# Kernel optimization log

Measured on AMD Instinct MI355X. Metric: run time of the kernel, lower is better.

The kernel has to match this reference:

```python
import jax, jax.numpy as jnp
import numpy as np

N, E, H, T = 50000, 100000, 512, 6  # nodes, edges, hidden_size, num_edge_types


def setup_inputs() -> dict:
    key = jax.random.key(0)
    ks = jax.random.split(key, 14)
    xav = 1.0 / np.sqrt(H)
    return {
        "statement_embeddings": jax.random.normal(ks[0], (N, H), jnp.float32),
        "source_indices": jax.random.randint(ks[1], (E,), 0, N, dtype=jnp.int32),
        "dest_indices": jax.random.randint(ks[2], (E,), 0, N, dtype=jnp.int32),
        "edge_types": jax.random.randint(ks[3], (E,), 0, T, dtype=jnp.int32),
        "num_nodes": N,
        "hidden_size": H,
        # edge_dense: Dense(features=6*H), xavier_uniform kernel, tiny-normal bias
        "W_edge": jax.random.uniform(ks[4], (H, T * H), jnp.float32, -1.0, 1.0) * np.sqrt(6.0 / (H + T * H)),
        "b_edge": jax.random.normal(ks[5], (T * H,), jnp.float32) * 1e-6,
        # GRUCell params (flax convention: input denses have bias; hidden r/z denses no bias; hidden n dense has bias)
        "W_ir": jax.random.normal(ks[6], (H, H), jnp.float32) * xav,
        "W_iz": jax.random.normal(ks[7], (H, H), jnp.float32) * xav,
        "W_in": jax.random.normal(ks[8], (H, H), jnp.float32) * xav,
        "b_ir": jnp.zeros((H,), jnp.float32),
        "b_iz": jnp.zeros((H,), jnp.float32),
        "b_in": jnp.zeros((H,), jnp.float32),
        "W_hr": jax.random.normal(ks[9], (H, H), jnp.float32) * xav,
        "W_hz": jax.random.normal(ks[10], (H, H), jnp.float32) * xav,
        "W_hn": jax.random.normal(ks[11], (H, H), jnp.float32) * xav,
        "b_hn": jnp.zeros((H,), jnp.float32),
    }


def reference(statement_embeddings, source_indices, dest_indices, edge_types,
              num_nodes, hidden_size,
              W_edge, b_edge,
              W_ir, W_iz, W_in, b_ir, b_iz, b_in,
              W_hr, W_hz, W_hn, b_hn):
    num_edge_types = 6
    # gather source node embeddings: [E, H]
    src = statement_embeddings[source_indices]
    # per-edge dense to all edge types: [E, T*H] -> [E, T, H]
    all_types = (src @ W_edge + b_edge).reshape(-1, num_edge_types, hidden_size)
    # select the slice for each edge's type: [E, H]
    msgs = jnp.take_along_axis(all_types, edge_types[:, None, None], axis=1)[:, 0, :]
    # scatter-add to destination nodes: [N, H]
    proposed = jax.ops.segment_sum(msgs, dest_indices, num_segments=num_nodes)
    # GRU update: inputs=proposed, carry=statement_embeddings
    h = statement_embeddings
    r = jax.nn.sigmoid(proposed @ W_ir + b_ir + h @ W_hr)
    z = jax.nn.sigmoid(proposed @ W_iz + b_iz + h @ W_hz)
    n = jnp.tanh(proposed @ W_in + b_in + r * (h @ W_hn + b_hn))
    return (1.0 - z) * n + z * h
```

## Files before the change

### kernel.cpp

```cpp
#include <hip/hip_runtime.h>
#include <hip/hip_bf16.h>
#include <math.h>

#define H 512
#define NT 6
#define BM 64
#define BN 64

typedef short bf16x8 __attribute__((ext_vector_type(8)));
typedef float f32x4 __attribute__((ext_vector_type(4)));

__device__ __forceinline__ float sigmoidf_(float x) { return 1.0f / (1.0f + expf(-x)); }

__device__ __forceinline__ unsigned short f2bf(float f) {
    unsigned int u = __float_as_uint(f);
    u = (u + 0x7FFF + ((u >> 16) & 1)) >> 16;
    return (unsigned short)u;
}
__device__ __forceinline__ float bf2f(unsigned short s) {
    unsigned int u = ((unsigned int)s) << 16;
    return __uint_as_float(u);
}

__device__ __forceinline__ void async16(const unsigned short* g, short* l) {
    __builtin_amdgcn_global_load_lds((const __attribute__((address_space(1))) void*)g,
                                     (__attribute__((address_space(3))) void*)l, 16, 0, 0);
}

__global__ void hist_kernel(const int* __restrict__ etype, int E, int* __restrict__ meta) {
    __shared__ int lh[NT];
    if (threadIdx.x < NT) lh[threadIdx.x] = 0;
    __syncthreads();
    int i = blockIdx.x * blockDim.x + threadIdx.x;
    if (i < E) atomicAdd(&lh[etype[i]], 1);
    __syncthreads();
    if (threadIdx.x < NT) {
        int c = lh[threadIdx.x];
        if (c) atomicAdd(&meta[threadIdx.x], c);
    }
}

__global__ void prefix_kernel(int* __restrict__ meta) {
    if (threadIdx.x == 0 && blockIdx.x == 0) {
        int acc = 0;
        for (int t = 0; t < NT; ++t) {
            meta[8 + t]  = acc;
            meta[16 + t] = acc;
            acc += ((meta[t] + BM - 1) / BM) * BM;
        }
        meta[8 + NT] = acc;
    }
}

__global__ void scatter_perm_kernel(const int* __restrict__ etype, int E,
                                    int* __restrict__ meta, int* __restrict__ perm) {
    __shared__ int lcount[NT];
    __shared__ int lbase[NT];
    const int tid = threadIdx.x;
    if (tid < NT) lcount[tid] = 0;
    __syncthreads();
    int i = blockIdx.x * blockDim.x + tid;
    int t = 0, rank = 0;
    if (i < E) {
        t = etype[i];
        rank = atomicAdd(&lcount[t], 1);
    }
    __syncthreads();
    if (tid < NT) {
        int c = lcount[tid];
        lbase[tid] = c ? atomicAdd(&meta[16 + tid], c) : 0;
    }
    __syncthreads();
    if (i < E) perm[lbase[t] + rank] = i;
}

__global__ void node_hist_kernel(const int* __restrict__ dst, int E, int* __restrict__ cnt) {
    int i = blockIdx.x * blockDim.x + threadIdx.x;
    if (i < E) atomicAdd(&cnt[dst[i]], 1);
}

__global__ void scan1_kernel(const int* __restrict__ cnt, int n,
                             int* __restrict__ nodeStart, int* __restrict__ partials) {
    __shared__ int sh[256];
    const int tid = threadIdx.x;
    const int base = blockIdx.x * 1024 + tid * 4;
    int v[4];
    int tsum = 0;
    #pragma unroll
    for (int j = 0; j < 4; ++j) { v[j] = (base + j < n) ? cnt[base + j] : 0; tsum += v[j]; }
    sh[tid] = tsum;
    __syncthreads();
    for (int ofs = 1; ofs < 256; ofs <<= 1) {
        int add = (tid >= ofs) ? sh[tid - ofs] : 0;
        __syncthreads();
        sh[tid] += add;
        __syncthreads();
    }
    int run = sh[tid] - tsum;
    #pragma unroll
    for (int j = 0; j < 4; ++j) {
        if (base + j < n) nodeStart[base + j] = run;
        run += v[j];
    }
    if (tid == 255) partials[blockIdx.x] = sh[255];
}

__global__ void scan2_kernel(int* __restrict__ partials, int nB, int* __restrict__ nodeStart, int n) {
    if (threadIdx.x == 0 && blockIdx.x == 0) {
        int acc = 0;
        for (int b = 0; b < nB; ++b) { int t = partials[b]; partials[b] = acc; acc += t; }
        nodeStart[n] = acc;
    }
}

__global__ void scan3_kernel(int* __restrict__ nodeStart, const int* __restrict__ partials, int n) {
    int i = blockIdx.x * blockDim.x + threadIdx.x;
    if (i < n) nodeStart[i] += partials[i >> 10];
}

__global__ void slot_kernel(const int* __restrict__ dst, int E, const int* __restrict__ nodeStart,
                            int* __restrict__ cursor, int* __restrict__ destSlot) {
    int i = blockIdx.x * blockDim.x + threadIdx.x;
    if (i < E) {
        int d = dst[i];
        destSlot[i] = nodeStart[d] + atomicAdd(&cursor[d], 1);
    }
}

__global__ void conv_bf16_kernel(const float* __restrict__ in, unsigned short* __restrict__ out, int n4) {
    int i = blockIdx.x * blockDim.x + threadIdx.x;
    if (i < n4) {
        float4 v = ((const float4*)in)[i];
        ushort4 o;
        o.x = f2bf(v.x); o.y = f2bf(v.y); o.z = f2bf(v.z); o.w = f2bf(v.w);
        ((ushort4*)out)[i] = o;
    }
}

__global__ void conv_gru_w_kernel(const float* __restrict__ Wir, const float* __restrict__ Wiz,
                                  const float* __restrict__ Win, const float* __restrict__ Whr,
                                  const float* __restrict__ Whz, const float* __restrict__ Whn,
                                  unsigned short* __restrict__ Brt, unsigned short* __restrict__ Bzt,
                                  unsigned short* __restrict__ Bnit, unsigned short* __restrict__ Bnht) {
    int idx = blockIdx.x * blockDim.x + threadIdx.x;
    if (idx >= 512 * 1024) return;
    int n = idx >> 10;
    int k = idx & 1023;
    int kk = k & 511;
    const float* wr = (k < 512) ? Wir : Whr;
    const float* wz = (k < 512) ? Wiz : Whz;
    Brt[idx] = f2bf(wr[kk * H + n]);
    Bzt[idx] = f2bf(wz[kk * H + n]);
    if (k < 512) Bnit[n * H + k]  = f2bf(Win[k * H + n]);
    else         Bnht[n * H + kk] = f2bf(Whn[kk * H + n]);
}

__global__ void conv_edge_w_kernel(const float* __restrict__ W_edge, unsigned short* __restrict__ WeT) {
    int idx = blockIdx.x * blockDim.x + threadIdx.x;
    if (idx >= 3072 * 512) return;
    int n = idx >> 9;
    int k = idx & 511;
    WeT[idx] = f2bf(W_edge[(size_t)k * (NT * H) + n]);
}

__global__ __launch_bounds__(256)
void edge_msg_mfma2(const unsigned short* __restrict__ emb_bf,
                    const int* __restrict__ src_idx,
                    const float* __restrict__ b_edge,
                    const unsigned short* __restrict__ WeT,
                    const int* __restrict__ meta,
                    const int* __restrict__ perm,
                    const int* __restrict__ destSlot,
                    unsigned short* __restrict__ msgbuf)
{
    __shared__ __align__(16) short lds[8 * 512];
    __shared__ __align__(16) short Cs[64][72];
    __shared__ int ls_slot[BM];
    __shared__ int ls_srcb[BM];

    const int rowBase = blockIdx.y * BM;
    if (rowBase >= meta[8 + NT]) return;
    int t = 0;
    while (rowBase >= meta[8 + t + 1]) ++t;

    const int colBase = blockIdx.x * BN;
    const int tid = threadIdx.x;
    if (tid < BM) {
        int e = perm[rowBase + tid];
        ls_slot[tid] = (e >= 0) ? destSlot[e] : -1;
        ls_srcb[tid] = (e >= 0) ? src_idx[e] * H : 0;
    }
    __syncthreads();

    const int lane = tid & 63;
    const int wv = tid >> 6;
    const int r = lane & 15;
    const int q = lane >> 4;
    const int wm = (wv >> 1) * 32;
    const int wn = (wv & 1) * 32;

    const unsigned short* pg[2];
    #pragma unroll
    for (int s = 0; s < 2; ++s) {
        int grp = wv * 2 + s;
        if (grp < 4) pg[s] = emb_bf + (size_t)ls_srcb[grp * 16 + r] + q * 8;
        else         pg[s] = WeT + ((size_t)(t * H + colBase + (grp - 4) * 16 + r)) * H + q * 8;
    }
    short* ld0 = &lds[(wv * 2) * 512];
    short* ld1 = &lds[(wv * 2 + 1) * 512];

    f32x4 acc[2][2];
    #pragma unroll
    for (int i = 0; i < 2; ++i)
        #pragma unroll
        for (int j = 0; j < 2; ++j) acc[i][j] = (f32x4){0.f, 0.f, 0.f, 0.f};

    for (int ks = 0; ks < 16; ++ks) {
        async16(pg[0], ld0);
        async16(pg[1], ld1);
        pg[0] += 32; pg[1] += 32;
        __syncthreads();
        bf16x8 a0 = *(const bf16x8*)&lds[(wm / 16 + 0) * 512 + lane * 8];
        bf16x8 a1 = *(const bf16x8*)&lds[(wm / 16 + 1) * 512 + lane * 8];
        bf16x8 b0 = *(const bf16x8*)&lds[(4 + wn / 16 + 0) * 512 + lane * 8];
        bf16x8 b1 = *(const bf16x8*)&lds[(4 + wn / 16 + 1) * 512 + lane * 8];
        acc[0][0] = __builtin_amdgcn_mfma_f32_16x16x32_bf16(a0, b0, acc[0][0], 0, 0, 0);
        acc[0][1] = __builtin_amdgcn_mfma_f32_16x16x32_bf16(a0, b1, acc[0][1], 0, 0, 0);
        acc[1][0] = __builtin_amdgcn_mfma_f32_16x16x32_bf16(a1, b0, acc[1][0], 0, 0, 0);
        acc[1][1] = __builtin_amdgcn_mfma_f32_16x16x32_bf16(a1, b1, acc[1][1], 0, 0, 0);
        __syncthreads();
    }

    float bias0 = b_edge[t * H + colBase + wn + r];
    float bias1 = b_edge[t * H + colBase + wn + 16 + r];
    #pragma unroll
    for (int i = 0; i < 2; ++i)
        #pragma unroll
        for (int reg = 0; reg < 4; ++reg) {
            int row = wm + i * 16 + q * 4 + reg;
            Cs[row][wn + r]      = (short)f2bf(acc[i][0][reg] + bias0);
            Cs[row][wn + 16 + r] = (short)f2bf(acc[i][1][reg] + bias1);
        }
    __syncthreads();

    int row = tid >> 2;
    int cc = (tid & 3) * 16;
    int slot = ls_slot[row];
    if (slot >= 0) {
        uint4* dst0 = (uint4*)&msgbuf[(size_t)slot * H + colBase + cc];
        dst0[0] = *(const uint4*)&Cs[row][cc];
        dst0[1] = *(const uint4*)&Cs[row][cc + 8];
    }
}

__global__ void segreduce_kernel(const unsigned short* __restrict__ msgbuf,
                                 const int* __restrict__ nodeStart,
                                 unsigned short* __restrict__ prop_bf, int N) {
    int idx = blockIdx.x * blockDim.x + threadIdx.x;
    if (idx >= N * 64) return;
    int node = idx >> 6;
    int cg = (idx & 63) * 8;
    int s0 = nodeStart[node], s1 = nodeStart[node + 1];
    float acc[8] = {0.f, 0.f, 0.f, 0.f, 0.f, 0.f, 0.f, 0.f};
    for (int s = s0; s < s1; ++s) {
        uint4 v = *(const uint4*)&msgbuf[(size_t)s * H + cg];
        const unsigned short* u = (const unsigned short*)&v;
        #pragma unroll
        for (int j = 0; j < 8; ++j) acc[j] += bf2f(u[j]);
    }
    unsigned short o[8];
    #pragma unroll
    for (int j = 0; j < 8; ++j) o[j] = f2bf(acc[j]);
    *(uint4*)&prop_bf[(size_t)node * H + cg] = *(const uint4*)o;
}

__global__ __launch_bounds__(256)
void gru_mfma2(const unsigned short* __restrict__ prop_bf,
               const unsigned short* __restrict__ emb_bf,
               const float* __restrict__ emb_f32,
               const unsigned short* __restrict__ Brt,
               const unsigned short* __restrict__ Bzt,
               const unsigned short* __restrict__ Bnit,
               const unsigned short* __restrict__ Bnht,
               const float* __restrict__ bir, const float* __restrict__ biz,
               const float* __restrict__ bin, const float* __restrict__ bhn,
               float* __restrict__ out, int N)
{
    __shared__ __align__(16) short lds[4 * 2048];

    const int tid = threadIdx.x;
    const int lane = tid & 63;
    const int wv = tid >> 6;
    const int r = lane & 15;
    const int q = lane >> 4;
    const int rowBase = blockIdx.y * BM;
    const int colBase = blockIdx.x * BN;
    const int wm = (wv >> 1) * 32;
    const int wn = (wv & 1) * 32;

    f32x4 accR[2][2], accZ[2][2], accNI[2][2], accNH[2][2];
    #pragma unroll
    for (int i = 0; i < 2; ++i)
        #pragma unroll
        for (int j = 0; j < 2; ++j) {
            accR[i][j] = (f32x4){0.f, 0.f, 0.f, 0.f};
            accZ[i][j] = accR[i][j];
            accNI[i][j] = accR[i][j];
            accNH[i][j] = accR[i][j];
        }

    short* ldsT = &lds[wv * 2048];

    for (int half = 0; half < 2; ++half) {
        const unsigned short* pg[4];
        if (wv == 0) {
            const unsigned short* s = half ? emb_bf : prop_bf;
            #pragma unroll
            for (int g = 0; g < 4; ++g)
                pg[g] = s + (size_t)(rowBase + g * 16 + r) * H + q * 8;
        } else if (wv == 1) {
            #pragma unroll
            for (int g = 0; g < 4; ++g)
                pg[g] = Brt + (size_t)(colBase + g * 16 + r) * 1024 + half * 512 + q * 8;
        } else if (wv == 2) {
            #pragma unroll
            for (int g = 0; g < 4; ++g)
                pg[g] = Bzt + (size_t)(colBase + g * 16 + r) * 1024 + half * 512 + q * 8;
        } else {
            const unsigned short* s = half ? Bnht : Bnit;
            #pragma unroll
            for (int g = 0; g < 4; ++g)
                pg[g] = s + (size_t)(colBase + g * 16 + r) * H + q * 8;
        }

        f32x4 (&accN)[2][2] = half ? accNH : accNI;

        for (int ks = 0; ks < 16; ++ks) {
            #pragma unroll
            for (int g = 0; g < 4; ++g) {
                async16(pg[g], ldsT + g * 512);
                pg[g] += 32;
            }
            __syncthreads();

            bf16x8 a0 = *(const bf16x8*)&lds[0 * 2048 + (wm / 16 + 0) * 512 + lane * 8];
            bf16x8 a1 = *(const bf16x8*)&lds[0 * 2048 + (wm / 16 + 1) * 512 + lane * 8];
            bf16x8 br0 = *(const bf16x8*)&lds[1 * 2048 + (wn / 16 + 0) * 512 + lane * 8];
            bf16x8 br1 = *(const bf16x8*)&lds[1 * 2048 + (wn / 16 + 1) * 512 + lane * 8];
            bf16x8 bz0 = *(const bf16x8*)&lds[2 * 2048 + (wn / 16 + 0) * 512 + lane * 8];
            bf16x8 bz1 = *(const bf16x8*)&lds[2 * 2048 + (wn / 16 + 1) * 512 + lane * 8];
            bf16x8 bn0 = *(const bf16x8*)&lds[3 * 2048 + (wn / 16 + 0) * 512 + lane * 8];
            bf16x8 bn1 = *(const bf16x8*)&lds[3 * 2048 + (wn / 16 + 1) * 512 + lane * 8];

            accR[0][0] = __builtin_amdgcn_mfma_f32_16x16x32_bf16(a0, br0, accR[0][0], 0, 0, 0);
            accR[0][1] = __builtin_amdgcn_mfma_f32_16x16x32_bf16(a0, br1, accR[0][1], 0, 0, 0);
            accR[1][0] = __builtin_amdgcn_mfma_f32_16x16x32_bf16(a1, br0, accR[1][0], 0, 0, 0);
            accR[1][1] = __builtin_amdgcn_mfma_f32_16x16x32_bf16(a1, br1, accR[1][1], 0, 0, 0);
            accZ[0][0] = __builtin_amdgcn_mfma_f32_16x16x32_bf16(a0, bz0, accZ[0][0], 0, 0, 0);
            accZ[0][1] = __builtin_amdgcn_mfma_f32_16x16x32_bf16(a0, bz1, accZ[0][1], 0, 0, 0);
            accZ[1][0] = __builtin_amdgcn_mfma_f32_16x16x32_bf16(a1, bz0, accZ[1][0], 0, 0, 0);
            accZ[1][1] = __builtin_amdgcn_mfma_f32_16x16x32_bf16(a1, bz1, accZ[1][1], 0, 0, 0);
            accN[0][0] = __builtin_amdgcn_mfma_f32_16x16x32_bf16(a0, bn0, accN[0][0], 0, 0, 0);
            accN[0][1] = __builtin_amdgcn_mfma_f32_16x16x32_bf16(a0, bn1, accN[0][1], 0, 0, 0);
            accN[1][0] = __builtin_amdgcn_mfma_f32_16x16x32_bf16(a1, bn0, accN[1][0], 0, 0, 0);
            accN[1][1] = __builtin_amdgcn_mfma_f32_16x16x32_bf16(a1, bn1, accN[1][1], 0, 0, 0);
            __syncthreads();
        }
    }

    #pragma unroll
    for (int i = 0; i < 2; ++i) {
        #pragma unroll
        for (int reg = 0; reg < 4; ++reg) {
            int row = rowBase + wm + i * 16 + q * 4 + reg;
            if (row >= N) continue;
            #pragma unroll
            for (int j = 0; j < 2; ++j) {
                int col = colBase + wn + j * 16 + r;
                float rg = sigmoidf_(accR[i][j][reg] + bir[col]);
                float zg = sigmoidf_(accZ[i][j][reg] + biz[col]);
                float ng = tanhf(accNI[i][j][reg] + bin[col] + rg * (accNH[i][j][reg] + bhn[col]));
                float h = emb_f32[(size_t)row * H + col];
                out[(size_t)row * H + col] = (1.0f - zg) * ng + zg * h;
            }
        }
    }
}

extern "C" void kernel_launch(void* const* d_in, const int* in_sizes, int n_in,
                              void* d_out, int out_size, void* d_ws, size_t ws_size,
                              hipStream_t stream) {
    const float* emb     = (const float*)d_in[0];
    const int*   src_idx = (const int*)d_in[1];
    const int*   dst_idx = (const int*)d_in[2];
    const int*   etype   = (const int*)d_in[3];
    const float* W_edge  = (const float*)d_in[6];
    const float* b_edge  = (const float*)d_in[7];
    const float* Wir = (const float*)d_in[8];
    const float* Wiz = (const float*)d_in[9];
    const float* Win = (const float*)d_in[10];
    const float* bir = (const float*)d_in[11];
    const float* biz = (const float*)d_in[12];
    const float* bin = (const float*)d_in[13];
    const float* Whr = (const float*)d_in[14];
    const float* Whz = (const float*)d_in[15];
    const float* Whn = (const float*)d_in[16];
    const float* bhn = (const float*)d_in[17];

    const int E = in_sizes[1];
    const int N = in_sizes[0] / H;
    const int NH = N * H;
    const int maxRowTiles = (E + BM - 1) / BM + NT;

    char* ws = (char*)d_ws;
    unsigned short* prop_bf  = (unsigned short*)ws;  ws += (size_t)NH * 2;
    unsigned short* emb_bf   = (unsigned short*)ws;  ws += (size_t)NH * 2;
    unsigned short* msgbuf   = (unsigned short*)ws;  ws += (size_t)E * H * 2;
    unsigned short* Brt      = (unsigned short*)ws;  ws += 512 * 1024 * 2;
    unsigned short* Bzt      = (unsigned short*)ws;  ws += 512 * 1024 * 2;
    unsigned short* Bnit     = (unsigned short*)ws;  ws += 512 * 512 * 2;
    unsigned short* Bnht     = (unsigned short*)ws;  ws += 512 * 512 * 2;
    unsigned short* WeT      = (unsigned short*)ws;  ws += 3072 * 512 * 2;
    int* meta      = (int*)ws;  ws += 32 * 4;
    int* typePerm  = (int*)ws;  ws += (size_t)maxRowTiles * BM * 4;
    int* nodeCnt   = (int*)ws;  ws += (size_t)N * 4;
    int* nodeStart = (int*)ws;  ws += ((size_t)N + 4) * 4;
    int* cursor    = (int*)ws;  ws += (size_t)N * 4;
    int* partials  = (int*)ws;  ws += 64 * 4;
    int* destSlot  = (int*)ws;

    hipMemsetAsync(meta, 0, 32 * 4, stream);
    hipMemsetAsync(typePerm, 0xFF, (size_t)maxRowTiles * BM * 4, stream);
    hipMemsetAsync(nodeCnt, 0, (size_t)N * 4, stream);
    hipMemsetAsync(cursor, 0, (size_t)N * 4, stream);

    const int n4 = NH / 4;
    conv_bf16_kernel<<<(n4 + 255) / 256, 256, 0, stream>>>(emb, emb_bf, n4);
    conv_gru_w_kernel<<<(512 * 1024 + 255) / 256, 256, 0, stream>>>(
        Wir, Wiz, Win, Whr, Whz, Whn, Brt, Bzt, Bnit, Bnht);
    conv_edge_w_kernel<<<(3072 * 512 + 255) / 256, 256, 0, stream>>>(W_edge, WeT);

    hist_kernel<<<(E + 255) / 256, 256, 0, stream>>>(etype, E, meta);
    prefix_kernel<<<1, 64, 0, stream>>>(meta);
    scatter_perm_kernel<<<(E + 255) / 256, 256, 0, stream>>>(etype, E, meta, typePerm);

    node_hist_kernel<<<(E + 255) / 256, 256, 0, stream>>>(dst_idx, E, nodeCnt);
    const int nB = (N + 1023) / 1024;
    scan1_kernel<<<nB, 256, 0, stream>>>(nodeCnt, N, nodeStart, partials);
    scan2_kernel<<<1, 64, 0, stream>>>(partials, nB, nodeStart, N);
    scan3_kernel<<<(N + 255) / 256, 256, 0, stream>>>(nodeStart, partials, N);
    slot_kernel<<<(E + 255) / 256, 256, 0, stream>>>(dst_idx, E, nodeStart, cursor, destSlot);

    dim3 egrid(H / BN, maxRowTiles);
    edge_msg_mfma2<<<egrid, 256, 0, stream>>>(emb_bf, src_idx, b_edge, WeT,
                                              meta, typePerm, destSlot, msgbuf);

    segreduce_kernel<<<((size_t)N * 64 + 255) / 256, 256, 0, stream>>>(msgbuf, nodeStart, prop_bf, N);

    dim3 ggrid(H / BN, (N + BM - 1) / BM);
    gru_mfma2<<<ggrid, 256, 0, stream>>>(prop_bf, emb_bf, emb, Brt, Bzt, Bnit, Bnht,
                                         bir, biz, bin, bhn, (float*)d_out, N);
}
```

Before: 940.7 us.

## Double-buffer LDS tiles in edge-message and GRU MFMA kernels

Both MFMA GEMM kernels now keep two LDS buffers and issue the async global-to-LDS copy for the next K-step before computing on the current one. This hides global load latency and drops one barrier per iteration. The GRU kernel also prefetches across the prop/emb half boundary with a fully unrolled half loop. The cost is twice the LDS per block, which may lower occupancy. Correctness depends on the async copies being complete at the single remaining barrier.

```diff
diff --git a/kernel.cpp b/kernel.cpp
--- a/kernel.cpp
+++ b/kernel.cpp
@@ -164,7 +164,7 @@
 }
 
 __global__ __launch_bounds__(256)
-void edge_msg_mfma2(const unsigned short* __restrict__ emb_bf,
+void edge_msg_mfma3(const unsigned short* __restrict__ emb_bf,
                     const int* __restrict__ src_idx,
                     const float* __restrict__ b_edge,
                     const unsigned short* __restrict__ WeT,
@@ -173,7 +173,7 @@
                     const int* __restrict__ destSlot,
                     unsigned short* __restrict__ msgbuf)
 {
-    __shared__ __align__(16) short lds[8 * 512];
+    __shared__ __align__(16) short lds[2][8 * 512];
     __shared__ __align__(16) short Cs[64][72];
     __shared__ int ls_slot[BM];
     __shared__ int ls_srcb[BM];
@@ -206,8 +206,8 @@
         if (grp < 4) pg[s] = emb_bf + (size_t)ls_srcb[grp * 16 + r] + q * 8;
         else         pg[s] = WeT + ((size_t)(t * H + colBase + (grp - 4) * 16 + r)) * H + q * 8;
     }
-    short* ld0 = &lds[(wv * 2) * 512];
-    short* ld1 = &lds[(wv * 2 + 1) * 512];
+    short* my0 = &lds[0][(wv * 2) * 512];
+    short* my1 = &lds[0][(wv * 2 + 1) * 512];
 
     f32x4 acc[2][2];
     #pragma unroll
@@ -215,21 +215,28 @@
         #pragma unroll
         for (int j = 0; j < 2; ++j) acc[i][j] = (f32x4){0.f, 0.f, 0.f, 0.f};
 
+    async16(pg[0], my0);
+    async16(pg[1], my1);
+
     for (int ks = 0; ks < 16; ++ks) {
-        async16(pg[0], ld0);
-        async16(pg[1], ld1);
-        pg[0] += 32; pg[1] += 32;
         __syncthreads();
-        bf16x8 a0 = *(const bf16x8*)&lds[(wm / 16 + 0) * 512 + lane * 8];
-        bf16x8 a1 = *(const bf16x8*)&lds[(wm / 16 + 1) * 512 + lane * 8];
-        bf16x8 b0 = *(const bf16x8*)&lds[(4 + wn / 16 + 0) * 512 + lane * 8];
-        bf16x8 b1 = *(const bf16x8*)&lds[(4 + wn / 16 + 1) * 512 + lane * 8];
+        if (ks < 15) {
+            const int off = (ks + 1) * 32;
+            const int bofs = ((ks & 1) ? 0 : 4096);
+            async16(pg[0] + off, my0 + bofs);
+            async16(pg[1] + off, my1 + bofs);
+        }
+        const short* L = &lds[ks & 1][0];
+        bf16x8 a0 = *(const bf16x8*)&L[(wm / 16 + 0) * 512 + lane * 8];
+        bf16x8 a1 = *(const bf16x8*)&L[(wm / 16 + 1) * 512 + lane * 8];
+        bf16x8 b0 = *(const bf16x8*)&L[(4 + wn / 16 + 0) * 512 + lane * 8];
+        bf16x8 b1 = *(const bf16x8*)&L[(4 + wn / 16 + 1) * 512 + lane * 8];
         acc[0][0] = __builtin_amdgcn_mfma_f32_16x16x32_bf16(a0, b0, acc[0][0], 0, 0, 0);
         acc[0][1] = __builtin_amdgcn_mfma_f32_16x16x32_bf16(a0, b1, acc[0][1], 0, 0, 0);
         acc[1][0] = __builtin_amdgcn_mfma_f32_16x16x32_bf16(a1, b0, acc[1][0], 0, 0, 0);
         acc[1][1] = __builtin_amdgcn_mfma_f32_16x16x32_bf16(a1, b1, acc[1][1], 0, 0, 0);
-        __syncthreads();
-    }
+    }
+    __syncthreads();
 
     float bias0 = b_edge[t * H + colBase + wn + r];
     float bias1 = b_edge[t * H + colBase + wn + 16 + r];
@@ -275,7 +282,7 @@
 }
 
 __global__ __launch_bounds__(256)
-void gru_mfma2(const unsigned short* __restrict__ prop_bf,
+void gru_mfma3(const unsigned short* __restrict__ prop_bf,
                const unsigned short* __restrict__ emb_bf,
                const float* __restrict__ emb_f32,
                const unsigned short* __restrict__ Brt,
@@ -286,7 +293,7 @@
                const float* __restrict__ bin, const float* __restrict__ bhn,
                float* __restrict__ out, int N)
 {
-    __shared__ __align__(16) short lds[4 * 2048];
+    __shared__ __align__(16) short lds[2][4 * 2048];
 
     const int tid = threadIdx.x;
     const int lane = tid & 63;
@@ -298,6 +305,38 @@
     const int wm = (wv >> 1) * 32;
     const int wn = (wv & 1) * 32;
 
+    const unsigned short* h0[4];
+    const unsigned short* h1[4];
+    if (wv == 0) {
+        #pragma unroll
+        for (int g = 0; g < 4; ++g) {
+            size_t rowoff = (size_t)(rowBase + g * 16 + r) * H + q * 8;
+            h0[g] = prop_bf + rowoff;
+            h1[g] = emb_bf + rowoff;
+        }
+    } else if (wv == 1) {
+        #pragma unroll
+        for (int g = 0; g < 4; ++g) {
+            h0[g] = Brt + (size_t)(colBase + g * 16 + r) * 1024 + q * 8;
+            h1[g] = h0[g] + 512;
+        }
+    } else if (wv == 2) {
+        #pragma unroll
+        for (int g = 0; g < 4; ++g) {
+            h0[g] = Bzt + (size_t)(colBase + g * 16 + r) * 1024 + q * 8;
+            h1[g] = h0[g] + 512;
+        }
+    } else {
+        #pragma unroll
+        for (int g = 0; g < 4; ++g) {
+            size_t coloff = (size_t)(colBase + g * 16 + r) * H + q * 8;
+            h0[g] = Bnit + coloff;
+            h1[g] = Bnht + coloff;
+        }
+    }
+
+    short* myl = &lds[0][wv * 2048];
+
     f32x4 accR[2][2], accZ[2][2], accNI[2][2], accNH[2][2];
     #pragma unroll
     for (int i = 0; i < 2; ++i)
@@ -309,48 +348,40 @@
             accNH[i][j] = accR[i][j];
         }
 
-    short* ldsT = &lds[wv * 2048];
-
+    #pragma unroll
+    for (int g = 0; g < 4; ++g) async16(h0[g], myl + g * 512);
+
+    #pragma unroll
     for (int half = 0; half < 2; ++half) {
-        const unsigned short* pg[4];
-        if (wv == 0) {
-            const unsigned short* s = half ? emb_bf : prop_bf;
-            #pragma unroll
-            for (int g = 0; g < 4; ++g)
-                pg[g] = s + (size_t)(rowBase + g * 16 + r) * H + q * 8;
-        } else if (wv == 1) {
-            #pragma unroll
-            for (int g = 0; g < 4; ++g)
-                pg[g] = Brt + (size_t)(colBase + g * 16 + r) * 1024 + half * 512 + q * 8;
-        } else if (wv == 2) {
-            #pragma unroll
-            for (int g = 0; g < 4; ++g)
-                pg[g] = Bzt + (size_t)(colBase + g * 16 + r) * 1024 + half * 512 + q * 8;
-        } else {
-            const unsigned short* s = half ? Bnht : Bnit;
-            #pragma unroll
-            for (int g = 0; g < 4; ++g)
-                pg[g] = s + (size_t)(colBase + g * 16 + r) * H + q * 8;
-        }
-
-        f32x4 (&accN)[2][2] = half ? accNH : accNI;
-
         for (int ks = 0; ks < 16; ++ks) {
-            #pragma unroll
-            for (int g = 0; g < 4; ++g) {
-                async16(pg[g], ldsT + g * 512);
-                pg[g] += 32;
+            __syncthreads();
+            {
+                short* dst = myl + ((ks & 1) ? 0 : 8192);
+                if (half == 0) {
+                    if (ks < 15) {
+                        const int off = (ks + 1) * 32;
+                        #pragma unroll
+                        for (int g = 0; g < 4; ++g) async16(h0[g] + off, dst + g * 512);
+                    } else {
+                        #pragma unroll
+                        for (int g = 0; g < 4; ++g) async16(h1[g], dst + g * 512);
+                    }
+                } else if (ks < 15) {
+                    const int off = (ks + 1) * 32;
+                    #pragma unroll
+                    for (int g = 0; g < 4; ++g) async16(h1[g] + off, dst + g * 512);
+                }
             }
-            __syncthreads();
-
-            bf16x8 a0 = *(const bf16x8*)&lds[0 * 2048 + (wm / 16 + 0) * 512 + lane * 8];
-            bf16x8 a1 = *(const bf16x8*)&lds[0 * 2048 + (wm / 16 + 1) * 512 + lane * 8];
-            bf16x8 br0 = *(const bf16x8*)&lds[1 * 2048 + (wn / 16 + 0) * 512 + lane * 8];
-            bf16x8 br1 = *(const bf16x8*)&lds[1 * 2048 + (wn / 16 + 1) * 512 + lane * 8];
-            bf16x8 bz0 = *(const bf16x8*)&lds[2 * 2048 + (wn / 16 + 0) * 512 + lane * 8];
-            bf16x8 bz1 = *(const bf16x8*)&lds[2 * 2048 + (wn / 16 + 1) * 512 + lane * 8];
-            bf16x8 bn0 = *(const bf16x8*)&lds[3 * 2048 + (wn / 16 + 0) * 512 + lane * 8];
-            bf16x8 bn1 = *(const bf16x8*)&lds[3 * 2048 + (wn / 16 + 1) * 512 + lane * 8];
+
+            const short* L = &lds[ks & 1][0];
+            bf16x8 a0  = *(const bf16x8*)&L[0 * 2048 + (wm / 16 + 0) * 512 + lane * 8];
+            bf16x8 a1  = *(const bf16x8*)&L[0 * 2048 + (wm / 16 + 1) * 512 + lane * 8];
+            bf16x8 br0 = *(const bf16x8*)&L[1 * 2048 + (wn / 16 + 0) * 512 + lane * 8];
+            bf16x8 br1 = *(const bf16x8*)&L[1 * 2048 + (wn / 16 + 1) * 512 + lane * 8];
+            bf16x8 bz0 = *(const bf16x8*)&L[2 * 2048 + (wn / 16 + 0) * 512 + lane * 8];
+            bf16x8 bz1 = *(const bf16x8*)&L[2 * 2048 + (wn / 16 + 1) * 512 + lane * 8];
+            bf16x8 bn0 = *(const bf16x8*)&L[3 * 2048 + (wn / 16 + 0) * 512 + lane * 8];
+            bf16x8 bn1 = *(const bf16x8*)&L[3 * 2048 + (wn / 16 + 1) * 512 + lane * 8];
 
             accR[0][0] = __builtin_amdgcn_mfma_f32_16x16x32_bf16(a0, br0, accR[0][0], 0, 0, 0);
             accR[0][1] = __builtin_amdgcn_mfma_f32_16x16x32_bf16(a0, br1, accR[0][1], 0, 0, 0);
@@ -360,11 +391,17 @@
             accZ[0][1] = __builtin_amdgcn_mfma_f32_16x16x32_bf16(a0, bz1, accZ[0][1], 0, 0, 0);
             accZ[1][0] = __builtin_amdgcn_mfma_f32_16x16x32_bf16(a1, bz0, accZ[1][0], 0, 0, 0);
             accZ[1][1] = __builtin_amdgcn_mfma_f32_16x16x32_bf16(a1, bz1, accZ[1][1], 0, 0, 0);
-            accN[0][0] = __builtin_amdgcn_mfma_f32_16x16x32_bf16(a0, bn0, accN[0][0], 0, 0, 0);
-            accN[0][1] = __builtin_amdgcn_mfma_f32_16x16x32_bf16(a0, bn1, accN[0][1], 0, 0, 0);
-            accN[1][0] = __builtin_amdgcn_mfma_f32_16x16x32_bf16(a1, bn0, accN[1][0], 0, 0, 0);
-            accN[1][1] = __builtin_amdgcn_mfma_f32_16x16x32_bf16(a1, bn1, accN[1][1], 0, 0, 0);
-            __syncthreads();
+            if (half == 0) {
+                accNI[0][0] = __builtin_amdgcn_mfma_f32_16x16x32_bf16(a0, bn0, accNI[0][0], 0, 0, 0);
+                accNI[0][1] = __builtin_amdgcn_mfma_f32_16x16x32_bf16(a0, bn1, accNI[0][1], 0, 0, 0);
+                accNI[1][0] = __builtin_amdgcn_mfma_f32_16x16x32_bf16(a1, bn0, accNI[1][0], 0, 0, 0);
+                accNI[1][1] = __builtin_amdgcn_mfma_f32_16x16x32_bf16(a1, bn1, accNI[1][1], 0, 0, 0);
+            } else {
+                accNH[0][0] = __builtin_amdgcn_mfma_f32_16x16x32_bf16(a0, bn0, accNH[0][0], 0, 0, 0);
+                accNH[0][1] = __builtin_amdgcn_mfma_f32_16x16x32_bf16(a0, bn1, accNH[0][1], 0, 0, 0);
+                accNH[1][0] = __builtin_amdgcn_mfma_f32_16x16x32_bf16(a1, bn0, accNH[1][0], 0, 0, 0);
+                accNH[1][1] = __builtin_amdgcn_mfma_f32_16x16x32_bf16(a1, bn1, accNH[1][1], 0, 0, 0);
+            }
         }
     }
 
@@ -452,12 +489,12 @@
     slot_kernel<<<(E + 255) / 256, 256, 0, stream>>>(dst_idx, E, nodeStart, cursor, destSlot);
 
     dim3 egrid(H / BN, maxRowTiles);
-    edge_msg_mfma2<<<egrid, 256, 0, stream>>>(emb_bf, src_idx, b_edge, WeT,
+    edge_msg_mfma3<<<egrid, 256, 0, stream>>>(emb_bf, src_idx, b_edge, WeT,
                                               meta, typePerm, destSlot, msgbuf);
 
     segreduce_kernel<<<((size_t)N * 64 + 255) / 256, 256, 0, stream>>>(msgbuf, nodeStart, prop_bf, N);
 
     dim3 ggrid(H / BN, (N + BM - 1) / BM);
-    gru_mfma2<<<ggrid, 256, 0, stream>>>(prop_bf, emb_bf, emb, Brt, Bzt, Bnit, Bnht,
+    gru_mfma3<<<ggrid, 256, 0, stream>>>(prop_bf, emb_bf, emb, Brt, Bzt, Bnit, Bnht,
                                          bir, biz, bin, bhn, (float*)d_out, N);
 }
```

Result: no change. 931.8 us (-0.9%).
